# Kernel optimization log

Hardware: AMD Instinct MI355X
Metric: run time of the kernel (lower is better)

The kernel has to match this reference:

```python
import math
import jax, jax.numpy as jnp
import numpy as np
from jax import lax

jax.config.update("jax_enable_x64", True)

DECOMP_LEVEL = 5
# Daubechies-5 (db5) decomposition low-pass filter (pywt convention)
_DB5_LO = np.array([0.003335725285001549, -0.012580751999015526, -0.006241490213011705,
                    0.07757149384006515, -0.03224486958502952, -0.24229488706619015,
                    0.13842814590110342, 0.7243085284385744, 0.6038292697974729,
                    0.160102397974125], dtype=np.float64)
_L = _DB5_LO.size
_DB5_HI = _DB5_LO[::-1].copy() * ((-1.0) ** np.arange(_L))  # QMF high-pass
LO = jnp.asarray(_DB5_LO, jnp.float32)
HI = jnp.asarray(_DB5_HI, jnp.float32)
LOR = jnp.asarray(_DB5_LO[::-1].copy(), jnp.float32)
HIR = jnp.asarray(_DB5_HI[::-1].copy(), jnp.float32)


def _an_last(x):
    # orthonormal periodized analysis along last axis: (..., n) -> (..., n/2) x2
    n = x.shape[-1]
    lead = x.shape[:-1]
    xp = jnp.concatenate([x, x[..., : _L - 2]], axis=-1).reshape(-1, 1, n + _L - 2)
    k = jnp.stack([LO, HI])[:, None, :]  # (2,1,L)
    y = lax.conv_general_dilated(xp, k, (2,), "VALID")  # (B,2,n/2)
    y = y.reshape(lead + (2, n // 2))
    return y[..., 0, :], y[..., 1, :]


def _syn_last(a, d):
    # exact transpose/inverse of _an_last (orthonormal -> W^T = W^-1)
    n2 = a.shape[-1]
    n = 2 * n2
    lead = a.shape[:-1]
    B = int(np.prod(lead)) if lead else 1
    u = jnp.zeros((B, 2, n), a.dtype)
    u = u.at[:, 0, ::2].set(a.reshape(B, n2))
    u = u.at[:, 1, ::2].set(d.reshape(B, n2))
    up = jnp.concatenate([u[..., -(_L - 1):], u], axis=-1)  # circular left pad
    k = jnp.stack([LOR, HIR])[None, :, :]  # (1,2,L)
    y = lax.conv_general_dilated(up, k, (1,), "VALID")  # (B,1,n)
    return y.reshape(lead + (n,))


def _dwt2(x):  # x: (C,h,w) -> ll, lh, hl, hh each (C,h/2,w/2)
    a_h, d_h = _an_last(x.swapaxes(-1, -2))
    a_h = a_h.swapaxes(-1, -2)
    d_h = d_h.swapaxes(-1, -2)
    ll, lh = _an_last(a_h)
    hl, hh = _an_last(d_h)
    return ll, lh, hl, hh


def _idwt2(ll, lh, hl, hh):
    a_h = _syn_last(ll, lh)
    d_h = _syn_last(hl, hh)
    return _syn_last(a_h.swapaxes(-1, -2), d_h.swapaxes(-1, -2)).swapaxes(-1, -2)


def _estimate_noise(data):
    p = data.shape[0]
    rr = data @ data.T
    rri = jnp.linalg.inv(rr + 1e-6 * jnp.eye(p, dtype=data.dtype))
    def per_band(i):
        xx = rri - jnp.outer(rri[:, i], rri[i, :]) / rri[i, i]
        beta = xx @ rr[:, i]
        return beta.at[i].set(0.0)
    betas = jax.vmap(per_band)(jnp.arange(p))  # (p,p)
    return data - betas @ data


def hyres_forward(x):
    H, W, K = x.shape
    N = H * W
    data = x.reshape(N, K).T.astype(jnp.float64)
    w = _estimate_noise(data)
    omega1 = (jnp.sqrt(jnp.var(w, axis=1, ddof=1)) + 1e-30) ** 2  # (K,) f64
    y_w = x * omega1 ** -0.5  # whitened, f64
    u, s, v_pca = jnp.linalg.svd(y_w.reshape(N, K), full_matrices=False)
    pc = (u * s).reshape(W, H, K).astype(jnp.float32).transpose(2, 0, 1)  # (K,H,W)
    # multi-level 2D DWT per channel
    ll = pc
    highs = []
    for _ in range(DECOMP_LEVEL):
        ll, lh, hl, hh = _dwt2(ll)
        highs.append((lh, hl, hh))
    # overwrite-style full coefficient image [[LL,LH],[HL,HH]] recursively
    full = ll
    for lh, hl, hh in reversed(highs):
        top = jnp.concatenate([full, lh], axis=-1)
        bot = jnp.concatenate([hl, hh], axis=-1)
        full = jnp.concatenate([top, bot], axis=-2)
    V = full.transpose(1, 2, 0).reshape(N, K)
    V2 = V * V
    norm_v = jnp.sum(V2)
    n_xyz = jnp.asarray(V.size, jnp.float32)
    col_norm = jnp.sum(V2, axis=0)  # (K,)
    # SURE of soft-threshold over a 15-point grid in [0, sqrt(log N)]
    ts = np.linspace(0.0, math.sqrt(math.log(N)), 15).astype(np.float32)
    sure_cols = []
    for t in ts:
        t2 = float(t * t)
        s_t = (jnp.sum(jnp.minimum(V2, t2), axis=0)
               + 2.0 * jnp.sum((V2 > t2).astype(jnp.float32), axis=0)
               - col_norm)
        sure_cols.append(s_t)
    sure_all = jnp.stack(sure_cols, axis=1)  # (K,15)
    c_const = norm_v - n_xyz
    # replicate the in-place cumulative update: S_r = sum_{j<r} S_j + sure_r + C
    def step(acc, sure_r):
        s_r = acc + sure_r + c_const
        return acc + s_r, jnp.min(s_r)
    _, min_sure = lax.scan(step, jnp.zeros((15,), jnp.float32), sure_all)
    # early-exit: first rank>1 where min_sure increases; else loop ends at K-1
    cond = min_sure[2:] > min_sure[1:-1]
    rank = jnp.where(jnp.any(cond), 2 + jnp.argmax(cond), K - 1)
    mask = (jnp.arange(K) < rank).astype(jnp.float32)[:, None, None]
    # truncation-to-rank == zeroing channels >= rank (inverse DWT is linear)
    y = ll * mask
    for lh, hl, hh in reversed(highs):
        y = _idwt2(y, lh * mask, hl * mask, hh * mask)
    y_est = y.transpose(1, 2, 0).reshape(N, K)  # zero cols beyond rank
    out = (omega1.astype(jnp.float32) ** 0.5) * (y_est @ v_pca.astype(jnp.float32)).reshape(H, W, K)
    return out


def setup_inputs() -> dict:
    key = jax.random.key(0)
    k1, k2, k3 = jax.random.split(key, 3)
    H = W = 384
    K = 191
    R = 8  # low-rank spectral structure + noise, as HyRes assumes
    a = jax.random.normal(k1, (H * W, R), jnp.float32)
    b = jax.random.normal(k2, (R, K), jnp.float32)
    x = (a @ b) / np.sqrt(R) + 0.1 * jax.random.normal(k3, (H * W, K), jnp.float32)
    return {"x": x.reshape(H, W, K)}


def reference(x):
    return hyres_forward(x)
```

## Files before the change

### kernel.cpp

```cpp
#include <hip/hip_runtime.h>
#include <math.h>

#define K_     191
#define LD     192
#define N_     147456
#define MSUB   16
#define NT     15
#define TRI_N  18336
#define SMEM_SZ ((TRI_N + 192 + 192 + 1056) * 8)
#define SMEM2_SZ (6880 * 8 + 32 * 4 + TRI_N * 4)

#define NPAIR  6
#define NSPLIT 128
#define CHUNK  (N_ / NSPLIT)
#define RSTEP  32

__constant__ float c_lo[10] = {
  0.003335725285001549f, -0.012580751999015526f, -0.006241490213011705f,
  0.07757149384006515f,  -0.03224486958502952f, -0.24229488706619015f,
  0.13842814590110342f,   0.7243085284385744f,   0.6038292697974729f,
  0.160102397974125f };
__constant__ float c_hi[10] = {
  0.160102397974125f,    -0.6038292697974729f,   0.7243085284385744f,
 -0.13842814590110342f,  -0.24229488706619015f,  0.03224486958502952f,
  0.07757149384006515f,   0.006241490213011705f,-0.012580751999015526f,
 -0.003335725285001549f };

__global__ __launch_bounds__(256) void k_colsum(const float* __restrict__ x,
                                                double* __restrict__ m)
{
  int t = threadIdx.x;
  long base = (long)blockIdx.x * 512;
  if (t < K_) {
    double s = 0.0;
    const float* p = x + base * K_ + t;
    for (int r = 0; r < 512; ++r) s += (double)p[(long)r * K_];
    atomicAdd(&m[t], s);
  }
}

__global__ __launch_bounds__(256, 3) void k_rr(const float* __restrict__ x,
                                               double* __restrict__ rrg)
{
  __shared__ double Asd[RSTEP][64];
  __shared__ double Bsd[RSTEP][64];

  const int bid   = blockIdx.x;
  const int split = bid & (NSPLIT - 1);
  const int pair  = bid >> 7;
  const int BI[6] = {0, 0, 0, 1, 1, 2};
  const int BJ[6] = {0, 1, 2, 1, 2, 2};
  const int bi = BI[pair], bj = BJ[pair];
  const int ca = bi * 64, cb = bj * 64;

  const int t  = threadIdx.x;
  const int tx = t & 15, ty = t >> 4;
  const long n0 = (long)split * CHUNK;

  double acc[4][4];
  #pragma unroll
  for (int v = 0; v < 4; ++v)
    #pragma unroll
    for (int u = 0; u < 4; ++u) acc[v][u] = 0.0;

  for (int r0 = 0; r0 < CHUNK; r0 += RSTEP) {
    for (int s = t; s < RSTEP * 16; s += 256) {
      int row = s >> 4, g = s & 15;
      long gr = (n0 + r0 + row) * (long)K_;
      int c4a = ca + g * 4, c4b = cb + g * 4;
      #pragma unroll
      for (int e = 0; e < 4; ++e) {
        Asd[row][g * 4 + e] = (c4a + e < K_) ? (double)x[gr + c4a + e] : 0.0;
        Bsd[row][g * 4 + e] = (c4b + e < K_) ? (double)x[gr + c4b + e] : 0.0;
      }
    }
    __syncthreads();
    #pragma unroll 4
    for (int k = 0; k < RSTEP; ++k) {
      double a0 = Asd[k][ty],      a1 = Asd[k][ty + 16];
      double a2 = Asd[k][ty + 32], a3 = Asd[k][ty + 48];
      double b0 = Bsd[k][tx],      b1 = Bsd[k][tx + 16];
      double b2 = Bsd[k][tx + 32], b3 = Bsd[k][tx + 48];
      acc[0][0] += a0 * b0; acc[0][1] += a0 * b1; acc[0][2] += a0 * b2; acc[0][3] += a0 * b3;
      acc[1][0] += a1 * b0; acc[1][1] += a1 * b1; acc[1][2] += a1 * b2; acc[1][3] += a1 * b3;
      acc[2][0] += a2 * b0; acc[2][1] += a2 * b1; acc[2][2] += a2 * b2; acc[2][3] += a2 * b3;
      acc[3][0] += a3 * b0; acc[3][1] += a3 * b1; acc[3][2] += a3 * b2; acc[3][3] += a3 * b3;
    }
    __syncthreads();
  }

  #pragma unroll
  for (int v = 0; v < 4; ++v) {
    int mrow = ca + ty + 16 * v;
    #pragma unroll
    for (int u = 0; u < 4; ++u) {
      int ncol = cb + tx + 16 * u;
      if (mrow < K_ && ncol < K_)
        atomicAdd(&rrg[(size_t)mrow * K_ + ncol], acc[v][u]);
    }
  }
}

__global__ __launch_bounds__(256) void k_reduce(const double* __restrict__ rrg,
                                                double* __restrict__ rr)
{
  int idx = blockIdx.x * 256 + threadIdx.x;
  if (idx >= TRI_N) return;
  int i = (int)((sqrtf(8.f * (float)idx + 1.f) - 1.f) * 0.5f);
  while ((i + 1) * (i + 2) / 2 <= idx) ++i;
  while (i * (i + 1) / 2 > idx) --i;
  int j = idx - (i * (i + 1)) / 2;
  double s = rrg[(size_t)j * K_ + i];
  rr[i * LD + j] = s;
  rr[j * LD + i] = s;
}

__global__ __launch_bounds__(1024) void k_small2(
    const double* __restrict__ rr, const double* __restrict__ m,
    double* __restrict__ invsq, float* __restrict__ sq32,
    float* __restrict__ normv)
{
  extern __shared__ double smem[];
  double* tri = smem;
  double* m_s = smem + TRI_N;
  double* w1  = m_s + 192;
  double* tmp = w1 + 192;
  const int t = threadIdx.x;
  __shared__ double spiv;

  if (t < K_) m_s[t] = m[t];
  for (int i = t >> 5; i < K_; i += 32) {
    int base = (i * (i + 1)) / 2;
    for (int j = t & 31; j <= i; j += 32) {
      double v = rr[i * LD + j];
      tri[base + j] = (i == j) ? v + 1e-6 : v;
    }
  }
  __syncthreads();

  for (int k = 0; k < K_; ++k) {
    if (t == 0) {
      double d = sqrt(tri[(k * (k + 1)) / 2 + k]);
      tri[(k * (k + 1)) / 2 + k] = d; spiv = d;
    }
    __syncthreads();
    double piv = spiv;
    for (int r = k + 1 + t; r < K_; r += 1024)
      tri[(r * (r + 1)) / 2 + k] /= piv;
    __syncthreads();
    {
      int tx = t & 31, ty = t >> 5;
      for (int r = k + 1 + ty; r < K_; r += 32) {
        int rb = (r * (r + 1)) / 2;
        double lrk = tri[rb + k];
        for (int c = k + 1 + tx; c <= r; c += 32)
          tri[rb + c] -= lrk * tri[(c * (c + 1)) / 2 + k];
      }
    }
    __syncthreads();
  }

  for (int J = 0; J < 6; ++J) {
    int j0 = J * 32;
    int nb = (K_ - j0 < 32) ? (K_ - j0) : 32;
    if (t < nb) {
      int c = t;
      for (int r = c; r < nb; ++r) {
        double s = (r == c) ? 1.0 : 0.0;
        int rb = ((j0 + r) * (j0 + r + 1)) / 2 + j0;
        for (int k = c; k < r; ++k) s -= tri[rb + k] * tmp[k * 33 + c];
        tmp[r * 33 + c] = s / tri[rb + r];
      }
    }
    __syncthreads();
    if (t < nb) {
      int c = t;
      for (int r = c; r < nb; ++r)
        tri[((j0 + r) * (j0 + r + 1)) / 2 + j0 + c] = tmp[r * 33 + c];
    }
    __syncthreads();
  }
  for (int J = 0; J < 5; ++J) {
    int j0 = J * 32;
    for (int I = J + 1; I < 6; ++I) {
      int i0 = I * 32;
      int nbi = (K_ - i0 < 32) ? (K_ - i0) : 32;
      int r = t & 31, c = t >> 5;
      double acc = 0.0;
      if (r < nbi) {
        int ri = i0 + r;
        int rb = (ri * (ri + 1)) / 2;
        for (int k = j0 + c; k < j0 + 32; ++k)
          acc += tri[rb + k] * tri[(k * (k + 1)) / 2 + j0 + c];
        for (int k = j0 + 32; k < i0; ++k)
          acc += tri[rb + k] * tri[(k * (k + 1)) / 2 + j0 + c];
      }
      tmp[r * 33 + c] = acc;
      __syncthreads();
      double out = 0.0;
      if (r < nbi) {
        int ri = i0 + r;
        int rb = (ri * (ri + 1)) / 2;
        for (int k = 0; k <= r; ++k)
          out -= tri[rb + i0 + k] * tmp[k * 33 + c];
        tri[rb + j0 + c] = out;
      }
      __syncthreads();
    }
  }

  if (t < K_) {
    int r = t, rb = (r * (r + 1)) / 2;
    double s = 0.0;
    for (int p = 0; p <= r; ++p) s += tri[rb + p] * m_s[p];
    w1[r] = s;
  }
  __syncthreads();
  if (t < K_) {
    int i = t;
    double s2 = 0.0, s1 = 0.0;
    for (int r = i; r < K_; ++r) {
      double xv = tri[(r * (r + 1)) / 2 + i];
      s2 += xv * xv;
      s1 += xv * w1[r];
    }
    double dii = s2;
    double q = 1.0 / dii;
    double sm_ = s1 / dii;
    double var = (q - sm_ * sm_ / (double)N_) / (double)(N_ - 1);
    double t1 = sqrt(var) + 1e-30;
    double om = t1 * t1;
    invsq[i] = 1.0 / sqrt(om);
    sq32[i] = sqrtf((float)om);
    tmp[i] = rr[i * LD + i] / om;
  }
  __syncthreads();
  if (t == 0) {
    double s = 0.0;
    for (int i = 0; i < K_; ++i) s += tmp[i];
    *normv = (float)s;
  }
}

__device__ __forceinline__ void cholqr(double* shQ, double* shS, int t)
{
  if (t < MSUB * MSUB) {
    int a = t & (MSUB - 1), b = t >> 4;
    double s = 0.0;
    for (int r = 0; r < K_; ++r) s += shQ[r * MSUB + a] * shQ[r * MSUB + b];
    shS[b * 17 + a] = s;
  }
  __syncthreads();
  for (int k = 0; k < MSUB; ++k) {
    if (t == 0) shS[k * 17 + k] = sqrt(shS[k * 17 + k]);
    __syncthreads();
    if (t > k && t < MSUB) shS[t * 17 + k] /= shS[k * 17 + k];
    __syncthreads();
    if (t < MSUB * MSUB) {
      int r = t & (MSUB - 1), c = t >> 4;
      if (c > k && r >= c) shS[r * 17 + c] -= shS[r * 17 + k] * shS[c * 17 + k];
    }
    __syncthreads();
  }
  if (t < K_) {
    double q[MSUB];
    #pragma unroll
    for (int c = 0; c < MSUB; ++c) {
      double v = shQ[t * MSUB + c];
      for (int p = 0; p < c; ++p) v -= q[p] * shS[c * 17 + p];
      q[c] = v / shS[c * 17 + c];
    }
    #pragma unroll
    for (int c = 0; c < MSUB; ++c) shQ[t * MSUB + c] = q[c];
  }
  __syncthreads();
}

__global__ __launch_bounds__(512) void k_sub(
    const double* __restrict__ rr, const double* __restrict__ invsq,
    float* __restrict__ W1, float* __restrict__ W2)
{
  extern __shared__ double dsm[];
  double* shQ  = dsm;
  double* shZ  = shQ + 3056;
  double* shS  = shZ + 3056;
  double* Ws   = shS + 272;
  double* inv_s= Ws + 272;
  double* ev   = inv_s + 192;
  double* cs_  = ev + 16;
  double* sn_  = cs_ + 8;
  int* ipp  = (int*)(sn_ + 8);
  int* iqq  = ipp + 8;
  int* perm = iqq + 8;
  float* tri = (float*)(perm + 16);
  const int t = threadIdx.x;

  if (t < K_) inv_s[t] = invsq[t];
  __syncthreads();
  for (int i = t >> 4; i < K_; i += 32) {
    int base = (i * (i + 1)) / 2;
    double di = inv_s[i];
    for (int j = t & 15; j <= i; j += 16)
      tri[base + j] = (float)(rr[i * LD + j] * di * inv_s[j]);
  }
  __syncthreads();

  for (int idx = t; idx < K_ * MSUB; idx += 512) {
    int i = idx >> 4, c = idx & 15;
    float g = (i >= c) ? tri[(i * (i + 1)) / 2 + c] : tri[(c * (c + 1)) / 2 + i];
    shQ[idx] = (double)g;
  }
  __syncthreads();

  cholqr(shQ, shS, t);
  for (int it = 0; it < 4; ++it) {
    for (int idx = t; idx < K_ * MSUB; idx += 512) shZ[idx] = shQ[idx];
    __syncthreads();
    for (int idx = t; idx < K_ * MSUB; idx += 512) {
      int i = idx >> 4, c = idx & 15;
      double s = 0.0;
      int rb = (i * (i + 1)) >> 1;
      for (int k = 0; k <= i; ++k) s += (double)tri[rb + k] * shZ[k * MSUB + c];
      int kk = ((i + 1) * (i + 2)) >> 1;
      for (int k = i + 1; k < K_; ++k) { s += (double)tri[kk + i] * shZ[k * MSUB + c]; kk += k + 1; }
      shQ[idx] = s;
    }
    __syncthreads();
    if (it < 3) cholqr(shQ, shS, t);
  }
  if (t < MSUB * MSUB) {
    int a = t & 15, b = t >> 4;
    double s = 0.0;
    for (int r = 0; r < K_; ++r) s += shZ[r * MSUB + b] * shQ[r * MSUB + a];
    shS[b * 17 + a] = s;
  }
  if (t < MSUB * 17) Ws[t] = 0.0;
  __syncthreads();
  if (t < MSUB) Ws[t * 17 + t] = 1.0;
  __syncthreads();
  for (int sweep = 0; sweep < 6; ++sweep) {
    for (int round = 0; round < 15; ++round) {
      if (t < 8) {
        int ia = (t == 0) ? 0 : (1 + ((t - 1 + round) % 15));
        int ib = 1 + ((14 - t + round) % 15);
        int p = ia < ib ? ia : ib;
        int q = ia < ib ? ib : ia;
        double app = shS[p * 17 + p], aqq = shS[q * 17 + q], apq = shS[p * 17 + q];
        double c = 1.0, s = 0.0;
        if (fabs(apq) > 1e-30 * (fabs(app) + fabs(aqq)) && apq != 0.0) {
          double tau = (aqq - app) / (2.0 * apq);
          double tt = (tau >= 0.0 ? 1.0 : -1.0) / (fabs(tau) + sqrt(1.0 + tau * tau));
          c = 1.0 / sqrt(1.0 + tt * tt); s = tt * c;
        }
        cs_[t] = c; sn_[t] = s; ipp[t] = p; iqq[t] = q;
      }
      __syncthreads();
      if (t < 128) {
        int i = t & 15, mI = t >> 4;
        int p = ipp[mI], q = iqq[mI];
        double c = cs_[mI], s = sn_[mI];
        double u = shS[i * 17 + p], v = shS[i * 17 + q];
        shS[i * 17 + p] = c * u - s * v; shS[i * 17 + q] = s * u + c * v;
        double wu = Ws[i * 17 + p], wv = Ws[i * 17 + q];
        Ws[i * 17 + p] = c * wu - s * wv; Ws[i * 17 + q] = s * wu + c * wv;
      }
      __syncthreads();
      if (t < 128) {
        int j = t & 15, mI = t >> 4;
        int p = ipp[mI], q = iqq[mI];
        double c = cs_[mI], s = sn_[mI];
        double u = shS[p * 17 + j], v = shS[q * 17 + j];
        shS[p * 17 + j] = c * u - s * v; shS[q * 17 + j] = s * u + c * v;
      }
      __syncthreads();
    }
  }
  if (t == 0) {
    for (int i = 0; i < MSUB; ++i) { ev[i] = shS[i * 17 + i]; perm[i] = i; }
    for (int i = 0; i < MSUB; ++i) {
      int best = i;
      for (int j = i + 1; j < MSUB; ++j)
        if (ev[perm[j]] > ev[perm[best]]) best = j;
      int tp = perm[i]; perm[i] = perm[best]; perm[best] = tp;
    }
  }
  __syncthreads();
  for (int idx = t; idx < K_ * MSUB; idx += 512) {
    int i = idx >> 4, c = idx & 15;
    int pc_ = perm[c];
    double e = 0.0;
    #pragma unroll
    for (int p = 0; p < MSUB; ++p) e += shZ[i * MSUB + p] * Ws[p * 17 + pc_];
    W1[i * MSUB + c] = (float)(inv_s[i] * e);
    W2[c * K_ + i]   = (float)(e / inv_s[i]);
  }
}

__global__ __launch_bounds__(256) void k_pc(const float* __restrict__ x,
                                            const float* __restrict__ W1,
                                            float* __restrict__ pc)
{
  __shared__ float xs[32][192];
  __shared__ float w1s[K_ * MSUB];
  int t = threadIdx.x;
  long n0 = (long)blockIdx.x * 32;
  for (int idx = t; idx < K_ * MSUB; idx += 256) w1s[idx] = W1[idx];
  for (int idx = t; idx < 32 * K_; idx += 256) {
    int row = idx / K_, col = idx - row * K_;
    xs[row][col] = x[(n0 + row) * K_ + col];
  }
  __syncthreads();
  int c = t & 15, nl = t >> 4;
  float a0 = 0.f, a1 = 0.f;
  for (int k = 0; k < K_; ++k) {
    float w = w1s[k * MSUB + c];
    a0 += xs[nl][k] * w;
    a1 += xs[nl + 16][k] * w;
  }
  __syncthreads();
  float* ts = &xs[0][0];
  ts[c * 33 + nl]      = a0;
  ts[c * 33 + nl + 16] = a1;
  __syncthreads();
  for (int idx = t; idx < MSUB * 32; idx += 256) {
    int cc = idx >> 5, nn = idx & 31;
    pc[(size_t)cc * N_ + n0 + nn] = ts[cc * 33 + nn];
  }
}

__global__ __launch_bounds__(256) void k_dwtv(const float* __restrict__ in,
                                              float* __restrict__ outv, int s)
{
  long gid = (long)blockIdx.x * 256 + threadIdx.x;
  int h = s >> 1;
  long per = (long)h * s;
  if (gid >= MSUB * per) return;
  int ch = (int)(gid / per);
  long rem = gid - (long)ch * per;
  int r = (int)(rem / s);
  int col = (int)(rem - (long)r * s);
  const float* cin = in + (long)ch * s * s;
  float la = 0.f, ld_ = 0.f;
  int base = 2 * r;
  #pragma unroll
  for (int l = 0; l < 10; ++l) {
    int rr_ = base + l; if (rr_ >= s) rr_ -= s;
    float v = cin[(long)rr_ * s + col];
    la += c_lo[l] * v; ld_ += c_hi[l] * v;
  }
  float* cout = outv + (long)ch * s * s;
  cout[(long)r * s + col] = la;
  cout[(long)(h + r) * s + col] = ld_;
}

__global__ __launch_bounds__(256) void k_dwth(const float* __restrict__ inv,
                                              float* __restrict__ llout,
                                              float* __restrict__ coef,
                                              int s, long offL, int last)
{
  long gid = (long)blockIdx.x * 256 + threadIdx.x;
  int h = s >> 1;
  long per = (long)s * h;
  if (gid >= MSUB * per) return;
  int ch = (int)(gid / per);
  long rem = gid - (long)ch * per;
  int r = (int)(rem / h);
  int mcol = (int)(rem - (long)r * h);
  const float* row = inv + (long)ch * s * s + (long)r * s;
  float lo = 0.f, hi = 0.f;
  int base = 2 * mcol;
  #pragma unroll
  for (int l = 0; l < 10; ++l) {
    int cc = base + l; if (cc >= s) cc -= s;
    float v = row[cc];
    lo += c_lo[l] * v; hi += c_hi[l] * v;
  }
  float* cslab = coef + (size_t)ch * N_ + offL;
  if (r < h) {
    llout[(size_t)ch * h * h + (long)r * h + mcol] = lo;
    if (last) coef[(size_t)ch * N_ + 147312 + (long)r * h + mcol] = lo;
    cslab[(long)r * h + mcol] = hi;
  } else {
    int rd = r - h;
    cslab[(long)h * h + (long)rd * h + mcol] = lo;
    cslab[(long)2 * h * h + (long)rd * h + mcol] = hi;
  }
}

__global__ __launch_bounds__(256) void k_stats(const float* __restrict__ coef,
                                               float* __restrict__ stats)
{
  int ch = blockIdx.x;
  int t = threadIdx.x;
  float T2[NT];
  {
    double stop = sqrt(log(147456.0));
    double step = stop / 14.0;
    for (int i = 0; i < NT; ++i) {
      double td = (i == 14) ? stop : (double)i * step;
      float tf = (float)td;
      T2[i] = tf * tf;
    }
  }
  float cn = 0.f, sm[NT], ct[NT];
  #pragma unroll
  for (int i = 0; i < NT; ++i) { sm[i] = 0.f; ct[i] = 0.f; }
  const float* base = coef + (size_t)ch * N_;
  for (int idx = t; idx < N_; idx += 256) {
    float v = base[idx];
    float v2 = v * v;
    cn += v2;
    #pragma unroll
    for (int i = 0; i < NT; ++i) {
      sm[i] += fminf(v2, T2[i]);
      ct[i] += (v2 > T2[i]) ? 1.0f : 0.0f;
    }
  }
  __shared__ float red[256];
  for (int a = 0; a < 31; ++a) {
    float val = (a == 0) ? cn : ((a < 16) ? sm[a - 1] : ct[a - 16]);
    red[t] = val;
    __syncthreads();
    for (int off = 128; off > 0; off >>= 1) {
      if (t < off) red[t] += red[t + off];
      __syncthreads();
    }
    if (t == 0) stats[ch * 31 + a] = red[0];
    __syncthreads();
  }
}

__global__ void k_rank(const float* __restrict__ stats,
                       const float* __restrict__ normv, int* __restrict__ rankp)
{
  if (threadIdx.x != 0 || blockIdx.x != 0) return;
  float c_const = *normv - 28164096.0f;
  float acc[NT];
  for (int i = 0; i < NT; ++i) acc[i] = 0.f;
  float minsure[MSUB];
  for (int r = 0; r < MSUB; ++r) {
    float cn = stats[r * 31 + 0];
    float mn = 3.4e38f;
    for (int i = 0; i < NT; ++i) {
      float sure = stats[r * 31 + 1 + i] + 2.0f * stats[r * 31 + 16 + i] - cn;
      float s_r = acc[i] + sure + c_const;
      acc[i] = acc[i] + s_r;
      if (s_r < mn) mn = s_r;
    }
    minsure[r] = mn;
  }
  int rank = -1;
  for (int r = 2; r < MSUB; ++r) {
    if (minsure[r] > minsure[r - 1]) { rank = r; break; }
  }
  if (rank < 0) rank = MSUB - 1;
  *rankp = rank;
}

__global__ __launch_bounds__(256) void k_out(const float* __restrict__ pc,
                                             const float* __restrict__ W2,
                                             const int* __restrict__ rankp,
                                             float* __restrict__ out)
{
  long gid = (long)blockIdx.x * 256 + threadIdx.x;
  int n = (int)(gid / K_);
  int j = (int)(gid - (long)n * K_);
  int rank = *rankp;
  float acc = 0.f;
  for (int c = 0; c < rank; ++c)
    acc += pc[(size_t)c * N_ + n] * W2[c * K_ + j];
  out[gid] = acc;
}

extern "C" void kernel_launch(void* const* d_in, const int* in_sizes, int n_in,
                              void* d_out, int out_size, void* d_ws, size_t ws_size,
                              hipStream_t stream)
{
  if (n_in < 1 || in_sizes[0] != N_ * K_) return;
  const float* x = (const float*)d_in[0];
  float* out = (float*)d_out;
  (void)out_size;

  char* w = (char*)d_ws;
  size_t off = 0;
  auto alloc = [&](size_t bytes) -> char* {
    char* p = w + off;
    off = (off + bytes + 255) & ~(size_t)255;
    return p;
  };
  double* m_    = (double*)alloc(K_ * 8);
  double* rrp   = (double*)alloc((size_t)K_ * K_ * 8);
  double* rr    = (double*)alloc((size_t)K_ * LD * 8);
  double* invsq = (double*)alloc(K_ * 8);
  float*  sq32  = (float*)alloc(K_ * 4);
  float*  normv = (float*)alloc(256);
  float*  W1    = (float*)alloc((size_t)K_ * MSUB * 4);
  float*  W2    = (float*)alloc((size_t)MSUB * K_ * 4);
  float*  pc    = (float*)alloc((size_t)MSUB * N_ * 4);
  float*  tmpv  = (float*)alloc((size_t)MSUB * N_ * 4);
  float*  coef  = (float*)alloc((size_t)MSUB * N_ * 4);
  float*  curA  = (float*)alloc((size_t)MSUB * 192 * 192 * 4);
  float*  curB  = (float*)alloc((size_t)MSUB * 96 * 96 * 4);
  float*  stats = (float*)alloc((size_t)MSUB * 31 * 4);
  int*    rankp = (int*)alloc(256);
  if (off > ws_size) return;

  hipMemsetAsync(m_, 0, K_ * sizeof(double), stream);
  hipMemsetAsync(rrp, 0, (size_t)K_ * K_ * sizeof(double), stream);

  hipFuncSetAttribute(reinterpret_cast<const void*>(k_small2),
                      hipFuncAttributeMaxDynamicSharedMemorySize, SMEM_SZ);
  hipFuncSetAttribute(reinterpret_cast<const void*>(k_sub),
                      hipFuncAttributeMaxDynamicSharedMemorySize, SMEM2_SZ);

  k_colsum<<<N_ / 512, 256, 0, stream>>>(x, m_);
  k_rr<<<NPAIR * NSPLIT, 256, 0, stream>>>(x, rrp);
  k_reduce<<<(TRI_N + 255) / 256, 256, 0, stream>>>(rrp, rr);
  k_small2<<<1, 1024, SMEM_SZ, stream>>>(rr, m_, invsq, sq32, normv);
  k_sub<<<1, 512, SMEM2_SZ, stream>>>(rr, invsq, W1, W2);
  k_pc<<<N_ / 32, 256, 0, stream>>>(x, W1, pc);

  int   sizes[5] = {384, 192, 96, 48, 24};
  long  offs[5]  = {0, 110592, 138240, 145152, 146880};
  float* lls[5]  = {curA, curB, curA, curB, curA};
  const float* curin = pc;
  for (int lev = 0; lev < 5; ++lev) {
    int s = sizes[lev], h = s >> 1;
    long nth = (long)MSUB * h * s;
    k_dwtv<<<(int)((nth + 255) / 256), 256, 0, stream>>>(curin, tmpv, s);
    k_dwth<<<(int)((nth + 255) / 256), 256, 0, stream>>>(tmpv, lls[lev], coef,
                                                         s, offs[lev],
                                                         lev == 4 ? 1 : 0);
    curin = lls[lev];
  }

  k_stats<<<MSUB, 256, 0, stream>>>(coef, stats);
  k_rank<<<1, 64, 0, stream>>>(stats, normv, rankp);
  k_out<<<(N_ * K_) / 256, 256, 0, stream>>>(pc, W2, rankp, out);
}
```

Measured before the change: 1.685 ms.

## Replace per-column Cholesky with blocked 32-wide panel factorization in k_small2

The 191x191 Cholesky factorization in shared memory used to run column by column with three barriers per column, which is 573 syncthreads in total. It now uses a blocked right-looking scheme: a 32x32 diagonal block is factored in registers with wave shuffles, the panel below is solved by triangular substitution per row, and the trailing matrix gets a 4x4-register-tiled rank-32 update. This cuts the barrier count to about 18 and raises arithmetic intensity. The cost is heavy register use from the 32-element double arrays, and the panel factorization is serialized within one wave.

```diff
diff --git a/kernel.cpp b/kernel.cpp
--- a/kernel.cpp
+++ b/kernel.cpp
@@ -126,7 +126,6 @@
   double* w1  = m_s + 192;
   double* tmp = w1 + 192;
   const int t = threadIdx.x;
-  __shared__ double spiv;
 
   if (t < K_) m_s[t] = m[t];
   for (int i = t >> 5; i < K_; i += 32) {
@@ -138,23 +137,114 @@
   }
   __syncthreads();
 
-  for (int k = 0; k < K_; ++k) {
-    if (t == 0) {
-      double d = sqrt(tri[(k * (k + 1)) / 2 + k]);
-      tri[(k * (k + 1)) / 2 + k] = d; spiv = d;
-    }
-    __syncthreads();
-    double piv = spiv;
-    for (int r = k + 1 + t; r < K_; r += 1024)
-      tri[(r * (r + 1)) / 2 + k] /= piv;
-    __syncthreads();
+  for (int J = 0; J < 6; ++J) {
+    const int j0 = J * 32;
+    const int nb = (K_ - j0 < 32) ? (K_ - j0) : 32;
+
+    if (t < 64) {
+      const int rl = t & 31;
+      double a[32];
+      #pragma unroll
+      for (int c = 0; c < 32; ++c) {
+        int i = j0 + rl;
+        a[c] = (c <= rl && rl < nb) ? tri[(i * (i + 1)) / 2 + j0 + c] : 0.0;
+      }
+      #pragma unroll
+      for (int k = 0; k < 32; ++k) {
+        double akk = __shfl(a[k], k);
+        double piv = sqrt(akk);
+        double inv = 1.0 / piv;
+        if (t == k) tmp[k] = inv;
+        a[k] = (rl == k) ? piv : a[k] * inv;
+        #pragma unroll
+        for (int c = k + 1; c < 32; ++c) {
+          double lck = __shfl(a[k], c);
+          if (c <= rl) a[c] -= a[k] * lck;
+        }
+      }
+      if (t < 32 && rl < nb) {
+        int i = j0 + rl;
+        int rb = (i * (i + 1)) / 2 + j0;
+        #pragma unroll
+        for (int c = 0; c < 32; ++c)
+          if (c <= rl) tri[rb + c] = a[c];
+      }
+    }
+    __syncthreads();
+
     {
-      int tx = t & 31, ty = t >> 5;
-      for (int r = k + 1 + ty; r < K_; r += 32) {
-        int rb = (r * (r + 1)) / 2;
-        double lrk = tri[rb + k];
-        for (int c = k + 1 + tx; c <= r; c += 32)
-          tri[rb + c] -= lrk * tri[(c * (c + 1)) / 2 + k];
+      int p = j0 + 32 + t;
+      if (nb == 32 && p < K_) {
+        int pb = (p * (p + 1)) / 2 + j0;
+        double v[32];
+        #pragma unroll
+        for (int c = 0; c < 32; ++c) v[c] = tri[pb + c];
+        #pragma unroll
+        for (int c = 0; c < 32; ++c) {
+          double s = v[c];
+          #pragma unroll
+          for (int q = 0; q < c; ++q) {
+            int cc = j0 + c;
+            s -= v[q] * tri[(cc * (cc + 1)) / 2 + j0 + q];
+          }
+          v[c] = s * tmp[c];
+        }
+        #pragma unroll
+        for (int c = 0; c < 32; ++c) tri[pb + c] = v[c];
+      }
+    }
+    __syncthreads();
+
+    {
+      int s0 = j0 + 32;
+      int n = K_ - s0;
+      if (n > 0) {
+        int R4 = (n + 3) >> 2;
+        int T4 = R4 * (R4 + 1) / 2;
+        for (int tile = t; tile < T4; tile += 1024) {
+          int ti = (int)((sqrtf(8.f * (float)tile + 1.f) - 1.f) * 0.5f);
+          while ((ti + 1) * (ti + 2) / 2 <= tile) ++ti;
+          while (ti * (ti + 1) / 2 > tile) --ti;
+          int tj = tile - ti * (ti + 1) / 2;
+          int r0 = s0 + ti * 4, c0 = s0 + tj * 4;
+          int rb[4], cb[4];
+          #pragma unroll
+          for (int u = 0; u < 4; ++u) {
+            int r = (r0 + u < K_) ? r0 + u : K_ - 1;
+            rb[u] = (r * (r + 1)) / 2;
+            int c = (c0 + u < K_) ? c0 + u : K_ - 1;
+            cb[u] = (c * (c + 1)) / 2;
+          }
+          double acc[4][4];
+          #pragma unroll
+          for (int u = 0; u < 4; ++u)
+            #pragma unroll
+            for (int v2 = 0; v2 < 4; ++v2) acc[u][v2] = 0.0;
+          #pragma unroll 4
+          for (int p = 0; p < 32; ++p) {
+            double lr[4], lc[4];
+            #pragma unroll
+            for (int u = 0; u < 4; ++u) {
+              lr[u] = tri[rb[u] + j0 + p];
+              lc[u] = tri[cb[u] + j0 + p];
+            }
+            #pragma unroll
+            for (int u = 0; u < 4; ++u)
+              #pragma unroll
+              for (int v2 = 0; v2 < 4; ++v2) acc[u][v2] += lr[u] * lc[v2];
+          }
+          #pragma unroll
+          for (int u = 0; u < 4; ++u) {
+            int r = r0 + u;
+            if (r < K_) {
+              #pragma unroll
+              for (int v2 = 0; v2 < 4; ++v2) {
+                int c = c0 + v2;
+                if (c <= r) tri[rb[u] + c] -= acc[u][v2];
+              }
+            }
+          }
+        }
       }
     }
     __syncthreads();
```

Result: no change. 1.663 ms (-1.3%).
